# Performance work log

Hardware: AMD Instinct MI355X
Metric: run time of the kernel (lower is better)

The kernel has to match this reference:

```python
import jax, jax.numpy as jnp
import numpy as np

B, T, S, D, H = 8, 512, 512, 512, 8
DH = D // H
EPS = 1e-5


def _ln(x, g, b):
    m = x.mean(-1, keepdims=True)
    v = x.var(-1, keepdims=True)
    return (x - m) / jnp.sqrt(v + EPS) * g + b


def setup_inputs() -> dict:
    key = jax.random.key(0)
    ks = jax.random.split(key, 24)
    w = lambda k, shp: (jax.random.normal(k, shp, jnp.float32) * 0.02)
    causal = jnp.where(jnp.tril(jnp.ones((T, T), bool)), 0.0, -1e9).astype(jnp.float32)
    return {
        "tgt": jax.random.normal(ks[0], (B, T, D), jnp.float32),
        "memory": jax.random.normal(ks[1], (B, S, D), jnp.float32),
        "tgt_mask": causal,
        "gate": jax.random.uniform(ks[2], (T, D), jnp.float32),
        # self-attn params (torch MultiheadAttention packed in_proj layout)
        "sa_in_w": w(ks[3], (3 * D, D)), "sa_in_b": w(ks[4], (3 * D,)),
        "sa_out_w": w(ks[5], (D, D)), "sa_out_b": w(ks[6], (D,)),
        # cross-attn params
        "ca_in_w": w(ks[7], (3 * D, D)), "ca_in_b": w(ks[8], (3 * D,)),
        "ca_out_w": w(ks[9], (D, D)), "ca_out_b": w(ks[10], (D,)),
        # FFN
        "ff1_w": w(ks[11], (4 * D, D)), "ff1_b": w(ks[12], (4 * D,)),
        "ff2_w": w(ks[13], (D, 4 * D)), "ff2_b": w(ks[14], (D,)),
        # layernorms
        "ln1_g": jnp.ones((D,), jnp.float32), "ln1_b": jnp.zeros((D,), jnp.float32),
        "ln2_g": jnp.ones((D,), jnp.float32), "ln2_b": jnp.zeros((D,), jnp.float32),
        "ln3_g": jnp.ones((D,), jnp.float32), "ln3_b": jnp.zeros((D,), jnp.float32),
    }


def reference(tgt, memory, tgt_mask, gate,
              sa_in_w, sa_in_b, sa_out_w, sa_out_b,
              ca_in_w, ca_in_b, ca_out_w, ca_out_b,
              ff1_w, ff1_b, ff2_w, ff2_b,
              ln1_g, ln1_b, ln2_g, ln2_b, ln3_g, ln3_b):
    b, t, d = tgt.shape
    s = memory.shape[1]
    scale = 1.0 / jnp.sqrt(jnp.float32(DH))

    # ---- self attention (standard batched MHA, additive mask) ----
    wq, wk, wv = jnp.split(sa_in_w, 3, axis=0)
    bq, bk, bv = jnp.split(sa_in_b, 3, axis=0)
    q = ((tgt @ wq.T + bq).reshape(b, t, H, DH)) * scale
    k = (tgt @ wk.T + bk).reshape(b, t, H, DH)
    v = (tgt @ wv.T + bv).reshape(b, t, H, DH)
    scores = jnp.einsum('bthd,bshd->bhts', q, k) + tgt_mask  # (B,H,T,T)
    attn = jax.nn.softmax(scores, axis=-1)
    sa = jnp.einsum('bhts,bshd->bthd', attn, v).reshape(b, t, d) @ sa_out_w.T + sa_out_b
    x = _ln(tgt + sa, ln1_g, ln1_b)

    # ---- gated cross attention ----
    # Original: key_{b,t,s} = W_k(gate_t * memory_{b,s}) + b_k materialized as (B*T,S,D).
    # Faithful refactor: distribute W_k, fold (q W_k) with gate into the query side.
    cwq, cwk, cwv = jnp.split(ca_in_w, 3, axis=0)
    cbq, cbk, cbv = jnp.split(ca_in_b, 3, axis=0)
    cq = ((x @ cwq.T + cbq).reshape(b, t, H, DH)) * scale          # (B,T,H,dh)
    wk_h = cwk.reshape(H, DH, d)                                    # (H,dh,D)
    qW = jnp.einsum('bthe,hed->bthd', cq, wk_h)                     # (B,T,H,D)
    cscores = jnp.einsum('bthd,td,bsd->bhts', qW, gate, memory)     # (B,H,T,S)
    bk_h = cbk.reshape(H, DH)
    cscores = cscores + jnp.einsum('bthe,he->bht', cq, bk_h)[..., None]
    cattn = jax.nn.softmax(cscores, axis=-1)
    cv = (memory @ cwv.T + cbv).reshape(b, s, H, DH)
    ca = jnp.einsum('bhts,bshe->bthe', cattn, cv).reshape(b, t, d) @ ca_out_w.T + ca_out_b
    x = _ln(x + ca, ln2_g, ln2_b)

    # ---- FFN ----
    ff = jax.nn.relu(x @ ff1_w.T + ff1_b) @ ff2_w.T + ff2_b
    return _ln(x + ff, ln3_g, ln3_b)
```

## Files before the change

### kernel.cpp

```cpp
#include <hip/hip_runtime.h>
#include <hip/hip_bf16.h>

#define BB 8
#define TT 512
#define SS 512
#define DD 512
#define HH 8

typedef __attribute__((ext_vector_type(8))) short bf16x8;
typedef __attribute__((ext_vector_type(4))) float f32x4;
typedef unsigned short u16;

__device__ __forceinline__ u16 f2b(float f) {
    __hip_bfloat16 h = __float2bfloat16(f);
    return *reinterpret_cast<u16*>(&h);
}
__device__ __forceinline__ float b2f(u16 v) {
    unsigned int u = ((unsigned int)v) << 16;
    return __builtin_bit_cast(float, u);
}
__device__ __forceinline__ void g2lds16(const void* g, void* l) {
    __builtin_amdgcn_global_load_lds(
        (const __attribute__((address_space(1))) void*)g,
        (__attribute__((address_space(3))) void*)l, 16, 0, 0);
}
template <int N> __device__ __forceinline__ void waitvm();
template <> __device__ __forceinline__ void waitvm<0>()  { asm volatile("s_waitcnt vmcnt(0)" ::: "memory"); }
template <> __device__ __forceinline__ void waitvm<4>()  { asm volatile("s_waitcnt vmcnt(4)" ::: "memory"); }
template <> __device__ __forceinline__ void waitvm<6>()  { asm volatile("s_waitcnt vmcnt(6)" ::: "memory"); }
template <> __device__ __forceinline__ void waitvm<8>()  { asm volatile("s_waitcnt vmcnt(8)" ::: "memory"); }
__device__ __forceinline__ void barrier_raw() {
    asm volatile("" ::: "memory");
    __builtin_amdgcn_s_barrier();
    asm volatile("" ::: "memory");
}

struct CastSegs {
    const float* s[9];
    u16* d[9];
    int cum[10];
};
__global__ __launch_bounds__(256) void cast_multi(CastSegs sg) {
    const int total = sg.cum[9];
    for (int i = blockIdx.x * 256 + threadIdx.x; i < total; i += gridDim.x * 256) {
        int k = 0;
#pragma unroll
        for (int j = 1; j < 9; ++j) k += (i >= sg.cum[j]);
        const int loc = i - sg.cum[k];
        float4 v = ((const float4*)sg.s[k])[loc];
        ushort4 u;
        u.x = f2b(v.x); u.y = f2b(v.y); u.z = f2b(v.z); u.w = f2b(v.w);
        ((ushort4*)sg.d[k])[loc] = u;
    }
}

__global__ __launch_bounds__(256) void wkt_kernel(const float* __restrict__ w,
                                                  u16* __restrict__ o) {
    const int idx = blockIdx.x * 256 + threadIdx.x;
    const int h = idx >> 15, d = (idx >> 6) & 511, e = idx & 63;
    o[idx] = f2b(w[(size_t)(512 + h * 64 + e) * 512 + d]);
}

template <int TM, int TN, bool RELU, bool GATE>
__global__ __launch_bounds__(256) void gemm_bf16(
    const u16* __restrict__ A, int lda, long az,
    const u16* __restrict__ Bw, int ldb, long bz,
    const float* __restrict__ bias, const float* __restrict__ biasB,
    const float* __restrict__ gate,
    u16* __restrict__ C, int ldo, long cz,
    int K, float alpha, float alphaB) {
    __shared__ __align__(16) u16 As[2][TM * 64];
    __shared__ __align__(16) u16 Bs[2][TN * 64];
    const int tid = threadIdx.x;
    const int wave = tid >> 6, lane = tid & 63;
    const int lm = lane & 15, lg = lane >> 4;
    const int wm = wave >> 1, wn = wave & 1;
    const int m0 = blockIdx.y * TM, n0 = blockIdx.x * TN;
    A += (size_t)blockIdx.z * az;
    Bw += (size_t)blockIdx.z * bz;
    C += (size_t)blockIdx.z * cz;
    constexpr int MI = TM / 32;
    constexpr int FN = TN / 32;
    constexpr int LPS = MI + FN;

    f32x4 acc[MI][FN];
#pragma unroll
    for (int mi = 0; mi < MI; ++mi)
#pragma unroll
        for (int ni = 0; ni < FN; ++ni) acc[mi][ni] = (f32x4){0.f, 0.f, 0.f, 0.f};

    const int srow = lane >> 3;
    const int sbyte = ((lane & 7) << 4) ^ (srow << 4);
    const int xk = (lm & 7) << 4;

    auto stage = [&](int buf, int kt) {
#pragma unroll
        for (int j = 0; j < MI; ++j) {
            const int r = wave * (TM / 4) + j * 8;
            g2lds16((const char*)(A + (size_t)(m0 + r + srow) * lda + kt) + sbyte,
                    (char*)As[buf] + (size_t)r * 128);
        }
#pragma unroll
        for (int j = 0; j < FN; ++j) {
            const int r = wave * (TN / 4) + j * 8;
            g2lds16((const char*)(Bw + (size_t)(n0 + r + srow) * ldb + kt) + sbyte,
                    (char*)Bs[buf] + (size_t)r * 128);
        }
    };

    stage(0, 0);
    const int NK = K >> 6;
    for (int t = 0; t < NK; ++t) {
        const int cur = t & 1;
        if (t + 1 < NK) { stage(cur ^ 1, (t + 1) << 6); waitvm<LPS>(); }
        else            { waitvm<0>(); }
        barrier_raw();
#pragma unroll
        for (int kh = 0; kh < 2; ++kh) {
            const int cb = kh * 64 + lg * 16;
            bf16x8 af[MI], bfr[FN];
#pragma unroll
            for (int mi = 0; mi < MI; ++mi) {
                const int row = wm * (TM / 2) + mi * 16 + lm;
                af[mi] = *(const bf16x8*)((const char*)As[cur] + row * 128 + (cb ^ xk));
            }
#pragma unroll
            for (int ni = 0; ni < FN; ++ni) {
                const int row = wn * (TN / 2) + ni * 16 + lm;
                bfr[ni] = *(const bf16x8*)((const char*)Bs[cur] + row * 128 + (cb ^ xk));
            }
#pragma unroll
            for (int mi = 0; mi < MI; ++mi)
#pragma unroll
                for (int ni = 0; ni < FN; ++ni)
                    acc[mi][ni] = __builtin_amdgcn_mfma_f32_16x16x32_bf16(
                        af[mi], bfr[ni], acc[mi][ni], 0, 0, 0);
        }
        barrier_raw();
    }

    const float* bp = blockIdx.z ? biasB : bias;
    const float al = blockIdx.z ? alphaB : alpha;
#pragma unroll
    for (int mi = 0; mi < MI; ++mi)
#pragma unroll
        for (int ni = 0; ni < FN; ++ni)
#pragma unroll
            for (int r = 0; r < 4; ++r) {
                const int m = m0 + wm * (TM / 2) + mi * 16 + lg * 4 + r;
                const int n = n0 + wn * (TN / 2) + ni * 16 + lm;
                float v = acc[mi][ni][r];
                if constexpr (GATE) v *= gate[(size_t)(m & 511) * 512 + n];
                else                v = (v + bp[n]) * al;
                if constexpr (RELU) v = fmaxf(v, 0.f);
                C[(size_t)m * ldo + n] = f2b(v);
            }
}

__global__ __launch_bounds__(256) void gemm_scores(
    const u16* __restrict__ QWp, const u16* __restrict__ membp,
    float* __restrict__ SC) {
    __shared__ __align__(16) u16 As[2][128 * 64];
    __shared__ __align__(16) u16 Bs[2][128 * 64];
    const int tid = threadIdx.x;
    const int wave = tid >> 6, lane = tid & 63;
    const int lm = lane & 15, lg = lane >> 4;
    const int wm = wave >> 1, wn = wave & 1;
    const int m0 = blockIdx.y * 128, n0 = blockIdx.x * 128;
    const int z = blockIdx.z, b = z >> 3, h = z & 7;
    const u16* A  = QWp + (size_t)b * TT * 4096 + h * 512;
    const u16* Bw = membp + (size_t)b * SS * 512;
    float* C = SC + ((size_t)z << 18);

    f32x4 acc[4][4];
#pragma unroll
    for (int mi = 0; mi < 4; ++mi)
#pragma unroll
        for (int ni = 0; ni < 4; ++ni) acc[mi][ni] = (f32x4){0.f, 0.f, 0.f, 0.f};

    const int srow = lane >> 3;
    const int sbyte = ((lane & 7) << 4) ^ (srow << 4);
    const int xk = (lm & 7) << 4;

    auto stage = [&](int buf, int kt) {
#pragma unroll
        for (int j = 0; j < 4; ++j) {
            const int r = wave * 32 + j * 8;
            g2lds16((const char*)(A + (size_t)(m0 + r + srow) * 4096 + kt) + sbyte,
                    (char*)As[buf] + (size_t)r * 128);
            g2lds16((const char*)(Bw + (size_t)(n0 + r + srow) * 512 + kt) + sbyte,
                    (char*)Bs[buf] + (size_t)r * 128);
        }
    };

    stage(0, 0);
    for (int t = 0; t < 8; ++t) {
        const int cur = t & 1;
        if (t + 1 < 8) { stage(cur ^ 1, (t + 1) << 6); waitvm<8>(); }
        else           { waitvm<0>(); }
        barrier_raw();
#pragma unroll
        for (int kh = 0; kh < 2; ++kh) {
            const int cb = kh * 64 + lg * 16;
            bf16x8 af[4], bfr[4];
#pragma unroll
            for (int mi = 0; mi < 4; ++mi) {
                const int row = wm * 64 + mi * 16 + lm;
                af[mi] = *(const bf16x8*)((const char*)As[cur] + row * 128 + (cb ^ xk));
            }
#pragma unroll
            for (int ni = 0; ni < 4; ++ni) {
                const int row = wn * 64 + ni * 16 + lm;
                bfr[ni] = *(const bf16x8*)((const char*)Bs[cur] + row * 128 + (cb ^ xk));
            }
#pragma unroll
            for (int mi = 0; mi < 4; ++mi)
#pragma unroll
                for (int ni = 0; ni < 4; ++ni)
                    acc[mi][ni] = __builtin_amdgcn_mfma_f32_16x16x32_bf16(
                        af[mi], bfr[ni], acc[mi][ni], 0, 0, 0);
        }
        barrier_raw();
    }
#pragma unroll
    for (int mi = 0; mi < 4; ++mi)
#pragma unroll
        for (int ni = 0; ni < 4; ++ni)
#pragma unroll
            for (int r = 0; r < 4; ++r) {
                const int m = m0 + wm * 64 + mi * 16 + lg * 4 + r;
                const int n = n0 + wn * 64 + ni * 16 + lm;
                C[(size_t)m * 512 + n] = acc[mi][ni][r];
            }
}

__global__ __launch_bounds__(256) void softmax_pv(
    const float* __restrict__ SC, const u16* __restrict__ CV,
    u16* __restrict__ out) {
    const int t0 = blockIdx.x * 64, h = blockIdx.y, b = blockIdx.z;
    const int tid = threadIdx.x, wave = tid >> 6, lane = tid & 63;
    const int lm = lane & 15, lg = lane >> 4;
    __shared__ __align__(16) u16 Vt[64 * 512];

    {
        const int sp = tid * 2;
#pragma unroll
        for (int c = 0; c < 8; ++c) {
            bf16x8 v0 = *(const bf16x8*)(CV + ((size_t)b * SS + sp) * 512 + h * 64 + c * 8);
            bf16x8 v1 = *(const bf16x8*)(CV + ((size_t)b * SS + sp + 1) * 512 + h * 64 + c * 8);
#pragma unroll
            for (int j = 0; j < 8; ++j) {
                const int d = c * 8 + j;
                const unsigned int pk = (unsigned int)(u16)v0[j] |
                                        ((unsigned int)(u16)v1[j] << 16);
                *(unsigned int*)((char*)Vt + ((d << 10) + ((sp * 2) ^ ((d & 7) << 4)))) = pk;
            }
        }
    }

    const int tw = t0 + wave * 16;
    const float* srow = SC + ((size_t)(b * 8 + h) << 18) + (size_t)(tw + lm) * 512 + lg * 8;
    float4 sa[16][2];
#pragma unroll
    for (int k = 0; k < 16; ++k) {
        sa[k][0] = *(const float4*)(srow + k * 32);
        sa[k][1] = *(const float4*)(srow + k * 32 + 4);
    }
    float mx = -3e38f;
#pragma unroll
    for (int k = 0; k < 16; ++k) {
        mx = fmaxf(mx, fmaxf(fmaxf(sa[k][0].x, sa[k][0].y), fmaxf(sa[k][0].z, sa[k][0].w)));
        mx = fmaxf(mx, fmaxf(fmaxf(sa[k][1].x, sa[k][1].y), fmaxf(sa[k][1].z, sa[k][1].w)));
    }
    mx = fmaxf(mx, __shfl_xor(mx, 16));
    mx = fmaxf(mx, __shfl_xor(mx, 32));
    float sum = 0.f;
    bf16x8 pb[16];
#pragma unroll
    for (int k = 0; k < 16; ++k) {
        float p0 = __expf(sa[k][0].x - mx), p1 = __expf(sa[k][0].y - mx);
        float p2 = __expf(sa[k][0].z - mx), p3 = __expf(sa[k][0].w - mx);
        float p4 = __expf(sa[k][1].x - mx), p5 = __expf(sa[k][1].y - mx);
        float p6 = __expf(sa[k][1].z - mx), p7 = __expf(sa[k][1].w - mx);
        sum += (p0 + p1 + p2 + p3) + (p4 + p5 + p6 + p7);
        pb[k][0] = (short)f2b(p0); pb[k][1] = (short)f2b(p1);
        pb[k][2] = (short)f2b(p2); pb[k][3] = (short)f2b(p3);
        pb[k][4] = (short)f2b(p4); pb[k][5] = (short)f2b(p5);
        pb[k][6] = (short)f2b(p6); pb[k][7] = (short)f2b(p7);
    }
    sum += __shfl_xor(sum, 16);
    sum += __shfl_xor(sum, 32);

    __syncthreads();

    f32x4 o[4];
#pragma unroll
    for (int nt = 0; nt < 4; ++nt) o[nt] = (f32x4){0.f, 0.f, 0.f, 0.f};
#pragma unroll
    for (int k = 0; k < 16; ++k) {
#pragma unroll
        for (int nt = 0; nt < 4; ++nt) {
            const int d = nt * 16 + lm;
            const bf16x8 vf = *(const bf16x8*)((const char*)Vt +
                ((d << 10) + ((k * 64 + lg * 16) ^ ((d & 7) << 4))));
            o[nt] = __builtin_amdgcn_mfma_f32_16x16x32_bf16(pb[k], vf, o[nt], 0, 0, 0);
        }
    }
#pragma unroll
    for (int r = 0; r < 4; ++r) {
        const float rs = __shfl(sum, lg * 4 + r);
        const float inv = 1.f / rs;
#pragma unroll
        for (int nt = 0; nt < 4; ++nt)
            out[(size_t)(b * TT + tw + lg * 4 + r) * DD + h * 64 + nt * 16 + lm] =
                f2b(o[nt][r] * inv);
    }
}

__global__ __launch_bounds__(256) void flash_self(const u16* __restrict__ QKV,
                                                  u16* __restrict__ out) {
    const int t0 = blockIdx.x * 64, h = blockIdx.y, b = blockIdx.z;
    const int tid = threadIdx.x, wave = tid >> 6, lane = tid & 63;
    const int lm = lane & 15, lg = lane >> 4;
    __shared__ __align__(16) u16 Ks[32 * 64];
    __shared__ __align__(16) u16 Vt[64][40];
    __shared__ __align__(16) u16 P[4][16][40];

    const int tw = t0 + wave * 16;
    const size_t qrow = (size_t)(b * TT + tw + lm) * 1536 + h * 64;
    bf16x8 qf[2];
    qf[0] = *(const bf16x8*)(QKV + qrow + lg * 8);
    qf[1] = *(const bf16x8*)(QKV + qrow + 32 + lg * 8);

    float m_run[4], l_run[4];
    f32x4 oacc[4];
#pragma unroll
    for (int r = 0; r < 4; ++r) { m_run[r] = -3e38f; l_run[r] = 0.f; }
#pragma unroll
    for (int nt = 0; nt < 4; ++nt) oacc[nt] = (f32x4){0.f, 0.f, 0.f, 0.f};

    const int srow = lane >> 3, sbyte = ((lane & 7) << 4) ^ (srow << 4);
    const int xk = (lm & 7) << 4;
    const int smax = t0 + 64;
    for (int s0 = 0; s0 < smax; s0 += 32) {
        if (s0) __syncthreads();
        g2lds16((const char*)(QKV + (size_t)(b * TT + s0 + wave * 8 + srow) * 1536 +
                              512 + h * 64) + sbyte,
                (char*)Ks + wave * 1024);
        {
            const int s = tid & 31, d0 = (tid >> 5) * 8;
            bf16x8 vv = *(const bf16x8*)(QKV + (size_t)(b * TT + s0 + s) * 1536 +
                                         1024 + h * 64 + d0);
#pragma unroll
            for (int j = 0; j < 8; ++j) Vt[d0 + j][s] = (u16)vv[j];
        }
        __syncthreads();
        if (s0 <= tw + 15) {
            f32x4 sc0 = (f32x4){0.f, 0.f, 0.f, 0.f};
            f32x4 sc1 = (f32x4){0.f, 0.f, 0.f, 0.f};
#pragma unroll
            for (int f = 0; f < 2; ++f) {
                const int cb = f * 64 + lg * 16;
                bf16x8 k0 = *(const bf16x8*)((const char*)Ks + lm * 128 + (cb ^ xk));
                bf16x8 k1 = *(const bf16x8*)((const char*)Ks + (16 + lm) * 128 + (cb ^ xk));
                sc0 = __builtin_amdgcn_mfma_f32_16x16x32_bf16(qf[f], k0, sc0, 0, 0, 0);
                sc1 = __builtin_amdgcn_mfma_f32_16x16x32_bf16(qf[f], k1, sc1, 0, 0, 0);
            }
            float sv0[4], sv1[4], tm[4];
#pragma unroll
            for (int r = 0; r < 4; ++r) {
                const int t = tw + lg * 4 + r;
                sv0[r] = sc0[r] * 0.125f + ((s0 + lm) <= t ? 0.f : -1e9f);
                sv1[r] = sc1[r] * 0.125f + ((s0 + 16 + lm) <= t ? 0.f : -1e9f);
                tm[r] = fmaxf(sv0[r], sv1[r]);
            }
#pragma unroll
            for (int off = 1; off < 16; off <<= 1)
#pragma unroll
                for (int r = 0; r < 4; ++r) tm[r] = fmaxf(tm[r], __shfl_xor(tm[r], off));
            float fac[4], rs[4];
#pragma unroll
            for (int r = 0; r < 4; ++r) {
                const float mn = fmaxf(m_run[r], tm[r]);
                fac[r] = __expf(m_run[r] - mn);
                m_run[r] = mn;
                const float p0 = __expf(sv0[r] - mn);
                const float p1 = __expf(sv1[r] - mn);
                P[wave][lg * 4 + r][lm] = f2b(p0);
                P[wave][lg * 4 + r][16 + lm] = f2b(p1);
                rs[r] = p0 + p1;
            }
#pragma unroll
            for (int off = 1; off < 16; off <<= 1)
#pragma unroll
                for (int r = 0; r < 4; ++r) rs[r] += __shfl_xor(rs[r], off);
#pragma unroll
            for (int r = 0; r < 4; ++r) l_run[r] = l_run[r] * fac[r] + rs[r];
#pragma unroll
            for (int nt = 0; nt < 4; ++nt)
#pragma unroll
                for (int r = 0; r < 4; ++r) oacc[nt][r] *= fac[r];
            const bf16x8 pf = *(const bf16x8*)&P[wave][lm][lg * 8];
#pragma unroll
            for (int nt = 0; nt < 4; ++nt) {
                const bf16x8 vf = *(const bf16x8*)&Vt[nt * 16 + lm][lg * 8];
                oacc[nt] = __builtin_amdgcn_mfma_f32_16x16x32_bf16(pf, vf, oacc[nt], 0, 0, 0);
            }
        }
    }
#pragma unroll
    for (int nt = 0; nt < 4; ++nt)
#pragma unroll
        for (int r = 0; r < 4; ++r)
            out[(size_t)(b * TT + tw + lg * 4 + r) * DD + h * 64 + nt * 16 + lm] =
                f2b(oacc[nt][r] / l_run[r]);
}

template <bool R1B>
__global__ __launch_bounds__(256) void add_ln(
    const void* __restrict__ R1v, const u16* __restrict__ R2,
    const float* __restrict__ g, const float* __restrict__ bta,
    float* __restrict__ outf, u16* __restrict__ outb) {
    const int row = blockIdx.x, tid = threadIdx.x;
    float x0, x1;
    if constexpr (R1B) {
        ushort2 a = ((const ushort2*)((const u16*)R1v + (size_t)row * DD))[tid];
        x0 = b2f(a.x); x1 = b2f(a.y);
    } else {
        float2 a = ((const float2*)((const float*)R1v + (size_t)row * DD))[tid];
        x0 = a.x; x1 = a.y;
    }
    ushort2 c = ((const ushort2*)(R2 + (size_t)row * DD))[tid];
    x0 += b2f(c.x); x1 += b2f(c.y);

    __shared__ float2 red[256];
    red[tid] = make_float2(x0 + x1, x0 * x0 + x1 * x1);
    __syncthreads();
#pragma unroll
    for (int o = 128; o > 0; o >>= 1) {
        if (tid < o) {
            red[tid].x += red[tid + o].x;
            red[tid].y += red[tid + o].y;
        }
        __syncthreads();
    }
    const float mean = red[0].x * (1.f / 512.f);
    const float var = red[0].y * (1.f / 512.f) - mean * mean;
    const float rstd = rsqrtf(var + 1e-5f);
    const int i = tid * 2;
    const float y0 = (x0 - mean) * rstd * g[i] + bta[i];
    const float y1 = (x1 - mean) * rstd * g[i + 1] + bta[i + 1];
    if (outf) ((float2*)(outf + (size_t)row * DD))[tid] = make_float2(y0, y1);
    if (outb) {
        ushort2 ub; ub.x = f2b(y0); ub.y = f2b(y1);
        ((ushort2*)(outb + (size_t)row * DD))[tid] = ub;
    }
}

extern "C" void kernel_launch(void* const* d_in, const int* in_sizes, int n_in,
                              void* d_out, int out_size, void* d_ws, size_t ws_size,
                              hipStream_t stream) {
    const float* tgt      = (const float*)d_in[0];
    const float* memory   = (const float*)d_in[1];
    const float* gate     = (const float*)d_in[3];
    const float* sa_in_w  = (const float*)d_in[4];
    const float* sa_in_b  = (const float*)d_in[5];
    const float* sa_out_w = (const float*)d_in[6];
    const float* sa_out_b = (const float*)d_in[7];
    const float* ca_in_w  = (const float*)d_in[8];
    const float* ca_in_b  = (const float*)d_in[9];
    const float* ca_out_w = (const float*)d_in[10];
    const float* ca_out_b = (const float*)d_in[11];
    const float* ff1_w    = (const float*)d_in[12];
    const float* ff1_b    = (const float*)d_in[13];
    const float* ff2_w    = (const float*)d_in[14];
    const float* ff2_b    = (const float*)d_in[15];
    const float* ln1_g    = (const float*)d_in[16];
    const float* ln1_b    = (const float*)d_in[17];
    const float* ln2_g    = (const float*)d_in[18];
    const float* ln2_b    = (const float*)d_in[19];
    const float* ln3_g    = (const float*)d_in[20];
    const float* ln3_b    = (const float*)d_in[21];

    u16* ws16     = (u16*)d_ws;
    u16* QKVb     = ws16;
    u16* sa_preb  = ws16 + 6291456;
    u16* PRJb     = ws16 + 8388608;
    u16* X1b      = ws16 + 10485760;
    u16* memb     = ws16 + 12582912;
    u16* CQb      = ws16 + 14680064;
    u16* CVb      = ws16 + 16777216;
    u16* QW       = ws16 + 18874368;
    u16* ca_preb  = ws16 + 35651584;
    u16* PRJ2b    = ws16 + 37748736;
    u16* X2b      = ws16 + 39845888;
    u16* HHb      = ws16 + 41943040;
    u16* F1b      = ws16 + 50331648;
    u16* Wreg     = ws16 + 52428800;
    u16* sa_in_wb = Wreg;
    u16* sa_out_wb= Wreg + 786432;
    u16* ca_wq_b  = Wreg + 1048576;
    u16* ca_wv_b  = Wreg + 1310720;
    u16* WkT      = Wreg + 1572864;
    u16* ca_out_wb= Wreg + 1835008;
    u16* ff1_wb   = Wreg + 2097152;
    u16* ff2_wb   = Wreg + 3145728;
    u16* tgtb     = ws16 + 56623104;
    float* SC     = (float*)(ws16 + 58720256);
    float* outf   = (float*)d_out;

    const dim3 blk(256);

    CastSegs sg;
    sg.s[0]=tgt; sg.s[1]=memory; sg.s[2]=sa_in_w; sg.s[3]=sa_out_w;
    sg.s[4]=ca_in_w; sg.s[5]=ca_in_w + (size_t)1024*512; sg.s[6]=ca_out_w;
    sg.s[7]=ff1_w; sg.s[8]=ff2_w;
    sg.d[0]=tgtb; sg.d[1]=memb; sg.d[2]=sa_in_wb; sg.d[3]=sa_out_wb;
    sg.d[4]=ca_wq_b; sg.d[5]=ca_wv_b; sg.d[6]=ca_out_wb;
    sg.d[7]=ff1_wb; sg.d[8]=ff2_wb;
    {
        const int n4[9] = {524288,524288,196608,65536,65536,65536,65536,262144,262144};
        int c = 0;
        for (int i = 0; i < 9; ++i) { sg.cum[i] = c; c += n4[i]; }
        sg.cum[9] = c;
    }
    cast_multi<<<2048, blk, 0, stream>>>(sg);
    wkt_kernel<<<1024, blk, 0, stream>>>(ca_in_w, WkT);

    gemm_bf16<128,128,false,false><<<dim3(12,32,1), blk, 0, stream>>>(
        tgtb,512,0, sa_in_wb,512,0, sa_in_b,sa_in_b,nullptr,
        QKVb,1536,0, 512, 1.f,1.f);
    flash_self<<<dim3(8,8,8), blk, 0, stream>>>(QKVb, sa_preb);
    gemm_bf16<64,64,false,false><<<dim3(8,64,1), blk, 0, stream>>>(
        sa_preb,512,0, sa_out_wb,512,0, sa_out_b,sa_out_b,nullptr,
        PRJb,512,0, 512, 1.f,1.f);
    add_ln<false><<<4096, blk, 0, stream>>>(tgt, PRJb, ln1_g, ln1_b, nullptr, X1b);
    gemm_bf16<64,64,false,false><<<dim3(8,64,2), blk, 0, stream>>>(
        X1b,512,2097152, ca_wq_b,512,262144, ca_in_b, ca_in_b+1024, nullptr,
        CQb,512,2097152, 512, 0.125f, 1.f);
    gemm_bf16<64,64,false,true><<<dim3(8,64,8), blk, 0, stream>>>(
        CQb,512,64, WkT,64,32768, nullptr,nullptr,gate,
        QW,4096,512, 64, 1.f,1.f);
    gemm_scores<<<dim3(4,4,64), blk, 0, stream>>>(QW, memb, SC);
    softmax_pv<<<dim3(8,8,8), blk, 0, stream>>>(SC, CVb, ca_preb);
    gemm_bf16<64,64,false,false><<<dim3(8,64,1), blk, 0, stream>>>(
        ca_preb,512,0, ca_out_wb,512,0, ca_out_b,ca_out_b,nullptr,
        PRJ2b,512,0, 512, 1.f,1.f);
    add_ln<true><<<4096, blk, 0, stream>>>(X1b, PRJ2b, ln2_g, ln2_b, nullptr, X2b);
    gemm_bf16<128,128,true,false><<<dim3(16,32,1), blk, 0, stream>>>(
        X2b,512,0, ff1_wb,512,0, ff1_b,ff1_b,nullptr,
        HHb,2048,0, 512, 1.f,1.f);
    gemm_bf16<64,64,false,false><<<dim3(8,64,1), blk, 0, stream>>>(
        HHb,2048,0, ff2_wb,2048,0, ff2_b,ff2_b,nullptr,
        F1b,512,0, 2048, 1.f,1.f);
    add_ln<true><<<4096, blk, 0, stream>>>(X2b, F1b, ln3_g, ln3_b, outf, nullptr);

    (void)in_sizes; (void)n_in; (void)out_size; (void)ws_size;
}
```

Baseline: 214.9 us.

## Split-K FFN2 with fp32 partials, XCD block swizzle, merge WkT cast kernel

The second FFN GEMM is split along K into two halves across blockIdx.z, each writing fp32 partial sums into the scores scratch buffer. A new add+LayerNorm kernel sums the residual, both partials and the bias. The change also remaps block indices so consecutive tiles land on the same XCD for better L2 locality, and folds the WkT transpose-cast into the multi-cast kernel to save one launch. Split-K doubles the block count for a GEMM that had only 512 tiles, at the cost of extra fp32 traffic for the partials.

```diff
diff --git a/kernel.cpp b/kernel.cpp
--- a/kernel.cpp
+++ b/kernel.cpp
@@ -34,11 +34,24 @@
     __builtin_amdgcn_s_barrier();
     asm volatile("" ::: "memory");
 }
+__device__ __forceinline__ void xcd_swz(int& bx, int& by, int& bz) {
+    const int gx = gridDim.x, gy = gridDim.y, gz = gridDim.z;
+    const int n = gx * gy * gz;
+    const int flat = bx + gx * (by + gy * bz);
+    const int q = n >> 3;
+    const int nf = (flat & 7) * q + (flat >> 3);
+    bx = nf % gx;
+    const int r = nf / gx;
+    by = r % gy;
+    bz = r / gy;
+}
 
 struct CastSegs {
     const float* s[9];
     u16* d[9];
     int cum[10];
+    const float* wsrc;
+    u16* wdst;
 };
 __global__ __launch_bounds__(256) void cast_multi(CastSegs sg) {
     const int total = sg.cum[9];
@@ -52,33 +65,32 @@
         u.x = f2b(v.x); u.y = f2b(v.y); u.z = f2b(v.z); u.w = f2b(v.w);
         ((ushort4*)sg.d[k])[loc] = u;
     }
-}
-
-__global__ __launch_bounds__(256) void wkt_kernel(const float* __restrict__ w,
-                                                  u16* __restrict__ o) {
-    const int idx = blockIdx.x * 256 + threadIdx.x;
-    const int h = idx >> 15, d = (idx >> 6) & 511, e = idx & 63;
-    o[idx] = f2b(w[(size_t)(512 + h * 64 + e) * 512 + d]);
-}
-
-template <int TM, int TN, bool RELU, bool GATE>
+    for (int idx = blockIdx.x * 256 + threadIdx.x; idx < 262144; idx += gridDim.x * 256) {
+        const int h = idx >> 15, d = (idx >> 6) & 511, e = idx & 63;
+        sg.wdst[idx] = f2b(sg.wsrc[(size_t)(512 + h * 64 + e) * 512 + d]);
+    }
+}
+
+template <int TM, int TN, bool RELU, bool GATE, typename OutT = u16, bool ADDBIAS = true>
 __global__ __launch_bounds__(256) void gemm_bf16(
     const u16* __restrict__ A, int lda, long az,
     const u16* __restrict__ Bw, int ldb, long bz,
     const float* __restrict__ bias, const float* __restrict__ biasB,
     const float* __restrict__ gate,
-    u16* __restrict__ C, int ldo, long cz,
+    OutT* __restrict__ C, int ldo, long cz,
     int K, float alpha, float alphaB) {
     __shared__ __align__(16) u16 As[2][TM * 64];
     __shared__ __align__(16) u16 Bs[2][TN * 64];
+    int bx = blockIdx.x, by = blockIdx.y, bzz = blockIdx.z;
+    xcd_swz(bx, by, bzz);
     const int tid = threadIdx.x;
     const int wave = tid >> 6, lane = tid & 63;
     const int lm = lane & 15, lg = lane >> 4;
     const int wm = wave >> 1, wn = wave & 1;
-    const int m0 = blockIdx.y * TM, n0 = blockIdx.x * TN;
-    A += (size_t)blockIdx.z * az;
-    Bw += (size_t)blockIdx.z * bz;
-    C += (size_t)blockIdx.z * cz;
+    const int m0 = by * TM, n0 = bx * TN;
+    A += (size_t)bzz * az;
+    Bw += (size_t)bzz * bz;
+    C += (size_t)bzz * cz;
     constexpr int MI = TM / 32;
     constexpr int FN = TN / 32;
     constexpr int LPS = MI + FN;
@@ -139,8 +151,8 @@
         barrier_raw();
     }
 
-    const float* bp = blockIdx.z ? biasB : bias;
-    const float al = blockIdx.z ? alphaB : alpha;
+    const float* bp = bzz ? biasB : bias;
+    const float al = bzz ? alphaB : alpha;
 #pragma unroll
     for (int mi = 0; mi < MI; ++mi)
 #pragma unroll
@@ -151,9 +163,10 @@
                 const int n = n0 + wn * (TN / 2) + ni * 16 + lm;
                 float v = acc[mi][ni][r];
                 if constexpr (GATE) v *= gate[(size_t)(m & 511) * 512 + n];
-                else                v = (v + bp[n]) * al;
+                else if constexpr (ADDBIAS) v = (v + bp[n]) * al;
                 if constexpr (RELU) v = fmaxf(v, 0.f);
-                C[(size_t)m * ldo + n] = f2b(v);
+                if constexpr (sizeof(OutT) == 2) C[(size_t)m * ldo + n] = (OutT)f2b(v);
+                else                             C[(size_t)m * ldo + n] = v;
             }
 }
 
@@ -162,12 +175,14 @@
     float* __restrict__ SC) {
     __shared__ __align__(16) u16 As[2][128 * 64];
     __shared__ __align__(16) u16 Bs[2][128 * 64];
+    int bx = blockIdx.x, by = blockIdx.y, bzz = blockIdx.z;
+    xcd_swz(bx, by, bzz);
     const int tid = threadIdx.x;
     const int wave = tid >> 6, lane = tid & 63;
     const int lm = lane & 15, lg = lane >> 4;
     const int wm = wave >> 1, wn = wave & 1;
-    const int m0 = blockIdx.y * 128, n0 = blockIdx.x * 128;
-    const int z = blockIdx.z, b = z >> 3, h = z & 7;
+    const int m0 = by * 128, n0 = bx * 128;
+    const int z = bzz, b = z >> 3, h = z & 7;
     const u16* A  = QWp + (size_t)b * TT * 4096 + h * 512;
     const u16* Bw = membp + (size_t)b * SS * 512;
     float* C = SC + ((size_t)z << 18);
@@ -455,6 +470,38 @@
         ushort2 ub; ub.x = f2b(y0); ub.y = f2b(y1);
         ((ushort2*)(outb + (size_t)row * DD))[tid] = ub;
     }
+}
+
+__global__ __launch_bounds__(256) void add_ln_sk(
+    const u16* __restrict__ X2, const float* __restrict__ P0,
+    const float* __restrict__ P1, const float* __restrict__ fb,
+    const float* __restrict__ g, const float* __restrict__ bta,
+    float* __restrict__ outf) {
+    const int row = blockIdx.x, tid = threadIdx.x;
+    ushort2 a = ((const ushort2*)(X2 + (size_t)row * DD))[tid];
+    float2 p0 = ((const float2*)(P0 + (size_t)row * DD))[tid];
+    float2 p1 = ((const float2*)(P1 + (size_t)row * DD))[tid];
+    const int i = tid * 2;
+    float x0 = b2f(a.x) + p0.x + p1.x + fb[i];
+    float x1 = b2f(a.y) + p0.y + p1.y + fb[i + 1];
+
+    __shared__ float2 red[256];
+    red[tid] = make_float2(x0 + x1, x0 * x0 + x1 * x1);
+    __syncthreads();
+#pragma unroll
+    for (int o = 128; o > 0; o >>= 1) {
+        if (tid < o) {
+            red[tid].x += red[tid + o].x;
+            red[tid].y += red[tid + o].y;
+        }
+        __syncthreads();
+    }
+    const float mean = red[0].x * (1.f / 512.f);
+    const float var = red[0].y * (1.f / 512.f) - mean * mean;
+    const float rstd = rsqrtf(var + 1e-5f);
+    const float y0 = (x0 - mean) * rstd * g[i] + bta[i];
+    const float y1 = (x1 - mean) * rstd * g[i + 1] + bta[i + 1];
+    ((float2*)(outf + (size_t)row * DD))[tid] = make_float2(y0, y1);
 }
 
 extern "C" void kernel_launch(void* const* d_in, const int* in_sizes, int n_in,
@@ -495,7 +542,6 @@
     u16* PRJ2b    = ws16 + 37748736;
     u16* X2b      = ws16 + 39845888;
     u16* HHb      = ws16 + 41943040;
-    u16* F1b      = ws16 + 50331648;
     u16* Wreg     = ws16 + 52428800;
     u16* sa_in_wb = Wreg;
     u16* sa_out_wb= Wreg + 786432;
@@ -518,6 +564,7 @@
     sg.d[0]=tgtb; sg.d[1]=memb; sg.d[2]=sa_in_wb; sg.d[3]=sa_out_wb;
     sg.d[4]=ca_wq_b; sg.d[5]=ca_wv_b; sg.d[6]=ca_out_wb;
     sg.d[7]=ff1_wb; sg.d[8]=ff2_wb;
+    sg.wsrc = ca_in_w; sg.wdst = WkT;
     {
         const int n4[9] = {524288,524288,196608,65536,65536,65536,65536,262144,262144};
         int c = 0;
@@ -525,7 +572,6 @@
         sg.cum[9] = c;
     }
     cast_multi<<<2048, blk, 0, stream>>>(sg);
-    wkt_kernel<<<1024, blk, 0, stream>>>(ca_in_w, WkT);
 
     gemm_bf16<128,128,false,false><<<dim3(12,32,1), blk, 0, stream>>>(
         tgtb,512,0, sa_in_wb,512,0, sa_in_b,sa_in_b,nullptr,
@@ -550,10 +596,11 @@
     gemm_bf16<128,128,true,false><<<dim3(16,32,1), blk, 0, stream>>>(
         X2b,512,0, ff1_wb,512,0, ff1_b,ff1_b,nullptr,
         HHb,2048,0, 512, 1.f,1.f);
-    gemm_bf16<64,64,false,false><<<dim3(8,64,1), blk, 0, stream>>>(
-        HHb,2048,0, ff2_wb,2048,0, ff2_b,ff2_b,nullptr,
-        F1b,512,0, 2048, 1.f,1.f);
-    add_ln<true><<<4096, blk, 0, stream>>>(X2b, F1b, ln3_g, ln3_b, outf, nullptr);
+    gemm_bf16<64,64,false,false,float,false><<<dim3(8,64,2), blk, 0, stream>>>(
+        HHb,2048,1024, ff2_wb,2048,1024, nullptr,nullptr,nullptr,
+        SC,512,2097152, 1024, 1.f,1.f);
+    add_ln_sk<<<4096, blk, 0, stream>>>(X2b, SC, SC + 2097152, ff2_b,
+                                        ln3_g, ln3_b, outf);
 
     (void)in_sizes; (void)n_in; (void)out_size; (void)ws_size;
 }
```

New measurement: 190.9 us. 1.13x faster.
